# Kernel tuning notes

Measured on AMD Instinct MI355X. Metric: run time of the kernel, lower is better.

Reference implementation:

```python
import jax, jax.numpy as jnp
import numpy as np

SIGMA = 3.0
TRUNCATE = 4.0          # scipy gaussian_filter default
THRESH = 0.01           # thresh_map_after_gaussian_filter
WIN = 5                 # weighted-average window
OFFSET = 0.4395         # offset_due_to_upsampling
SCORE_THRESH = 0.8


def _conv2d(x4, k4, pad):
    # x4: [M,1,H,W], k4: [1,1,kh,kw], pad: ((ph,ph),(pw,pw)) zero padding
    return jax.lax.conv_general_dilated(
        x4, k4, window_strides=(1, 1), padding=pad,
        dimension_numbers=('NCHW', 'OIHW', 'NCHW'))


def _gaussian_filter(x4):
    # scipy.ndimage.gaussian_filter(sigma=3, mode='reflect') == separable conv
    # with symmetric (edge-mirrored) padding, radius = int(truncate*sigma+0.5)
    r = int(TRUNCATE * SIGMA + 0.5)  # 12 -> 25-tap kernel
    t = jnp.arange(-r, r + 1, dtype=x4.dtype)
    k = jnp.exp(-(t * t) / (2.0 * SIGMA * SIGMA))
    k = k / k.sum()
    # along H
    xp = jnp.pad(x4, ((0, 0), (0, 0), (r, r), (0, 0)), mode='symmetric')
    x4 = _conv2d(xp, k.reshape(1, 1, -1, 1), ((0, 0), (0, 0)))
    # along W
    xp = jnp.pad(x4, ((0, 0), (0, 0), (0, 0), (r, r)), mode='symmetric')
    return _conv2d(xp, k.reshape(1, 1, 1, -1), ((0, 0), (0, 0)))


def setup_inputs() -> dict:
    key = jax.random.key(0)
    belief_maps = jax.random.uniform(key, (32, 16, 256, 256), dtype=jnp.float32)
    return {"belief_maps": belief_maps}


def reference(belief_maps):
    B, N, H, W = belief_maps.shape
    M = B * N
    m_ori = belief_maps.reshape(M, 1, H, W)

    # 1) gaussian smoothing for NMS
    g = _gaussian_filter(m_ori)[:, 0]  # [M,H,W]

    # 2) 4-neighbor local-maximum test (zero borders, exactly as numpy shifts)
    up    = jnp.pad(g, ((0, 0), (1, 0), (0, 0)))[:, :H, :]   # g[i-1,j], 0 at top
    down  = jnp.pad(g, ((0, 0), (0, 1), (0, 0)))[:, 1:, :]   # g[i+1,j], 0 at bottom
    left  = jnp.pad(g, ((0, 0), (0, 0), (1, 0)))[:, :, :W]   # g[i,j-1], 0 at left
    right = jnp.pad(g, ((0, 0), (0, 0), (0, 1)))[:, :, 1:]   # g[i,j+1], 0 at right
    peaks = (g >= up) & (g >= down) & (g >= left) & (g >= right) & (g > THRESH)

    # 3) weighted 5x5 window averages over the ORIGINAL map (zero-weight OOB)
    rows = jnp.arange(H, dtype=belief_maps.dtype)[:, None]
    cols = jnp.arange(W, dtype=belief_maps.dtype)[None, :]
    box = jnp.ones((1, 1, WIN, WIN), belief_maps.dtype)
    pad = ((WIN // 2, WIN // 2), (WIN // 2, WIN // 2))
    S  = _conv2d(m_ori, box, pad)[:, 0]                 # sum of weights
    SY = _conv2d(m_ori * rows, box, pad)[:, 0]          # sum(row * w)
    SX = _conv2d(m_ori * cols, box, pad)[:, 0]          # sum(col * w)

    m = m_ori[:, 0]
    neg_inf = jnp.array(-jnp.inf, belief_maps.dtype)
    masked = jnp.where(peaks, m, neg_inf).reshape(M, H * W)
    idx = jnp.argmax(masked, axis=1)                    # best-scoring peak per map
    npk = peaks.reshape(M, H * W).sum(axis=1)           # number of peaks

    def _take(a):
        return jnp.take_along_axis(a.reshape(M, H * W), idx[:, None], axis=1)[:, 0]

    score = _take(m)
    Ssum = _take(S)
    row_p = (idx // W).astype(belief_maps.dtype)
    col_p = (idx % W).astype(belief_maps.dtype)
    safe = jnp.where(Ssum == 0, jnp.ones_like(Ssum), Ssum)
    # try/except fallback to raw peak coords when all window weights are zero
    x = jnp.where(Ssum == 0, col_p, _take(SX) / safe) + OFFSET
    y = jnp.where(Ssum == 0, row_p, _take(SY) / safe) + OFFSET

    # single peak -> always valid; multiple peaks -> top score must be >= 0.8
    valid = (npk == 1) | ((npk > 1) & (score >= SCORE_THRESH))
    kx = jnp.where(valid, x, jnp.full_like(x, -999.999))
    ky = jnp.where(valid, y, jnp.full_like(y, -999.999))
    conf = valid.astype(belief_maps.dtype)
    return jnp.stack([kx, ky, conf], axis=-1).reshape(B, N, 3)
```

## Files before the change

kernel.cpp:

```cpp
#include <hip/hip_runtime.h>
#include <cmath>

#define HH 256
#define WW 256
#define RAD 12
#define KLEN 25
#define NMAPS 512
#define ESTRIP 32
#define NSTRIP (HH / ESTRIP)
#define RING 29

typedef float v2f __attribute__((ext_vector_type(2)));

__global__ __launch_bounds__(256) void blur_peak_strip(
    const float* __restrict__ in,
    float* __restrict__ sval,
    int* __restrict__ sidx,
    int* __restrict__ scnt)
{
    __shared__ __align__(16) float vrow[4][2][WW + 2 * RAD];

    const int tid  = threadIdx.x;
    const int l    = tid & 63;
    const int wv   = tid >> 6;
    const int sid  = blockIdx.x * 4 + wv;
    const int m     = sid >> 3;
    const int strip = sid & 7;
    const float4* map4 = reinterpret_cast<const float4*>(in) + (size_t)m * (HH * WW / 4);

    const int e0 = strip * ESTRIP;
    const int o0 = e0 - 1;

    float kf[KLEN];
    {
        float s = 0.f; float h[RAD + 1];
#pragma unroll
        for (int i = 0; i <= RAD; ++i) {
            float tt = (float)(i - RAD);
            h[i] = expf(-(tt * tt) / 18.0f);
            s += (i < RAD) ? 2.f * h[i] : h[i];
        }
#pragma unroll
        for (int i = 0; i <= RAD; ++i) h[i] /= s;
#pragma unroll
        for (int i = 0; i < KLEN; ++i) kf[i] = h[(i <= RAD) ? i : (2 * RAD - i)];
    }

    v2f rxy[RING], rzw[RING];
#pragma unroll
    for (int i = 0; i < RING; ++i) {
        int q = o0 + i - RAD;
        int r = (q < 0) ? (-q - 1) : q;
        float4 t4 = map4[(size_t)r * (WW / 4) + l];
        rxy[i] = (v2f){t4.x, t4.y};
        rzw[i] = (v2f){t4.z, t4.w};
    }

    float4 g0v  = make_float4(0.f, 0.f, 0.f, 0.f);
    float4 gm1v = g0v, gm2v = g0v;
    float bval = -1.f;
    int   bidx = 0x7FFFFFFF;
    int   cnt  = 0;
    float4 pf0, pf1, pf2, pf3, pf4;

#define PREFETCH(TT)                                                          \
    {                                                                         \
        int rb = o0 + 5 * (TT) + 17;                                          \
        int r0 = rb, r1 = rb + 1, r2 = rb + 2, r3 = rb + 3, r4 = rb + 4;      \
        if (r0 > HH - 1) r0 = 2 * HH - 1 - r0;                                \
        if (r1 > HH - 1) r1 = 2 * HH - 1 - r1;                                \
        if (r2 > HH - 1) r2 = 2 * HH - 1 - r2;                                \
        if (r3 > HH - 1) r3 = 2 * HH - 1 - r3;                                \
        if (r4 > HH - 1) r4 = 2 * HH - 1 - r4;                                \
        pf0 = map4[(size_t)r0 * (WW / 4) + l];                                \
        pf1 = map4[(size_t)r1 * (WW / 4) + l];                                \
        pf2 = map4[(size_t)r2 * (WW / 4) + l];                                \
        pf3 = map4[(size_t)r3 * (WW / 4) + l];                                \
        pf4 = map4[(size_t)r4 * (WW / 4) + l];                                \
    }

#define ROTATE()                                                              \
    {                                                                         \
        _Pragma("unroll")                                                     \
        for (int i = 0; i < RING - 5; ++i) {                                  \
            rxy[i] = rxy[i + 5]; rzw[i] = rzw[i + 5];                         \
        }                                                                     \
        rxy[24] = (v2f){pf0.x, pf0.y}; rzw[24] = (v2f){pf0.z, pf0.w};         \
        rxy[25] = (v2f){pf1.x, pf1.y}; rzw[25] = (v2f){pf1.z, pf1.w};         \
        rxy[26] = (v2f){pf2.x, pf2.y}; rzw[26] = (v2f){pf2.z, pf2.w};         \
        rxy[27] = (v2f){pf3.x, pf3.y}; rzw[27] = (v2f){pf3.z, pf3.w};         \
        rxy[28] = (v2f){pf4.x, pf4.y}; rzw[28] = (v2f){pf4.z, pf4.w};         \
    }

#define VCW(PP, TP)                                                           \
    {                                                                         \
        v2f vxyA = (v2f){0.f, 0.f}, vxyB = (v2f){0.f, 0.f};                   \
        v2f vzwA = (v2f){0.f, 0.f}, vzwB = (v2f){0.f, 0.f};                   \
        _Pragma("unroll")                                                     \
        for (int d = 0; d < KLEN; d += 2) {                                   \
            vxyA += kf[d] * rxy[(PP) + d];                                    \
            vzwA += kf[d] * rzw[(PP) + d];                                    \
        }                                                                     \
        _Pragma("unroll")                                                     \
        for (int d = 1; d < KLEN; d += 2) {                                   \
            vxyB += kf[d] * rxy[(PP) + d];                                    \
            vzwB += kf[d] * rzw[(PP) + d];                                    \
        }                                                                     \
        v2f vxy = vxyA + vxyB;                                                \
        v2f vzw = vzwA + vzwB;                                                \
        float* wb = vrow[wv][(TP) & 1];                                       \
        reinterpret_cast<float4*>(wb + RAD)[l] =                              \
            make_float4(vxy.x, vxy.y, vzw.x, vzw.y);                          \
        if (l < 3)   reinterpret_cast<float4*>(wb)[2 - l]   =                 \
            make_float4(vzw.y, vzw.x, vxy.y, vxy.x);                          \
        if (l >= 61) reinterpret_cast<float4*>(wb)[130 - l] =                 \
            make_float4(vzw.y, vzw.x, vxy.y, vxy.x);                          \
    }

#define HC()                                                                  \
    {                                                                         \
        float acc0 = 0.f, acc1 = 0.f, acc2 = 0.f, acc3 = 0.f;                 \
        const float4 rda[7] = {rd0, rd1, rd2, rd3, rd4, rd5, rd6};            \
        _Pragma("unroll")                                                     \
        for (int k = 0; k < 7; ++k) {                                         \
            _Pragma("unroll")                                                 \
            for (int e = 0; e < 4; ++e) {                                     \
                const int i = 4 * k + e;                                      \
                const float wval = (e == 0) ? rda[k].x : (e == 1) ? rda[k].y  \
                                 : (e == 2) ? rda[k].z : rda[k].w;            \
                if (i <= 24)           acc0 += kf[i]     * wval;              \
                if (i >= 1 && i <= 25) acc1 += kf[i - 1] * wval;              \
                if (i >= 2 && i <= 26) acc2 += kf[i - 2] * wval;              \
                if (i >= 3)            acc3 += kf[i - 3] * wval;              \
            }                                                                 \
        }                                                                     \
        gm2v = gm1v; gm1v = g0v;                                              \
        g0v = make_float4(acc0, acc1, acc2, acc3);                            \
    }

#define EV(SLOT, EROW)                                                        \
    {                                                                         \
        const int erow = (EROW);                                              \
        float lf0 = __shfl_up(gm1v.w, 1);   if (l == 0)  lf0 = 0.f;           \
        float rt3 = __shfl_down(gm1v.x, 1); if (l == 63) rt3 = 0.f;           \
        const bool etop = (erow == 0), ebot = (erow == HH - 1);               \
        const float gm1a[4] = {gm1v.x, gm1v.y, gm1v.z, gm1v.w};               \
        const float gm2a[4] = {gm2v.x, gm2v.y, gm2v.z, gm2v.w};               \
        const float g0a[4]  = {g0v.x,  g0v.y,  g0v.z,  g0v.w};                \
        const float mva[4]  = {rxy[SLOT].x, rxy[SLOT].y,                      \
                               rzw[SLOT].x, rzw[SLOT].y};                     \
        _Pragma("unroll")                                                     \
        for (int q = 0; q < 4; ++q) {                                         \
            float gE = gm1a[q];                                               \
            float up = etop ? 0.f : gm2a[q];                                  \
            float dn = ebot ? 0.f : g0a[q];                                   \
            float lf = (q == 0) ? lf0 : gm1a[q - 1];                          \
            float rt = (q == 3) ? rt3 : gm1a[q + 1];                          \
            float mx = fmaxf(fmaxf(up, dn), fmaxf(lf, rt));                   \
            bool pk = (gE >= mx) && (gE > 0.01f);                             \
            cnt += pk ? 1 : 0;                                                \
            float mv = mva[q];                                                \
            int fi = erow * WW + 4 * l + q;                                   \
            bool upd = pk && (mv > bval);                                     \
            bval = upd ? mv : bval;                                           \
            bidx = upd ? fi : bidx;                                           \
        }                                                                     \
    }

#define ROW_FULL(TB, PP)                                                      \
    {                                                                         \
        const int tpar = ((TB) + (PP)) & 1;      \
        const float4* rb4 =                                                   \
            reinterpret_cast<const float4*>(vrow[wv][tpar ^ 1]);              \
        float4 rd0 = rb4[l + 0], rd1 = rb4[l + 1], rd2 = rb4[l + 2],          \
               rd3 = rb4[l + 3], rd4 = rb4[l + 4], rd5 = rb4[l + 5],          \
               rd6 = rb4[l + 6];                                              \
        VCW(PP, tpar);                                                        \
        __builtin_amdgcn_wave_barrier();                                      \
        HC();                                                                 \
        EV((PP) + 10, o0 + 5 * (TB) + (PP) - 2);                              \
    }

#define ROW_NOEV(PP)                                                          \
    {                                                                         \
        const int tpar = (PP) & 1;                                            \
        const float4* rb4 =                                                   \
            reinterpret_cast<const float4*>(vrow[wv][tpar ^ 1]);              \
        float4 rd0 = rb4[l + 0], rd1 = rb4[l + 1], rd2 = rb4[l + 2],          \
               rd3 = rb4[l + 3], rd4 = rb4[l + 4], rd5 = rb4[l + 5],          \
               rd6 = rb4[l + 6];                                              \
        VCW(PP, PP);                                                          \
        __builtin_amdgcn_wave_barrier();                                      \
        HC();                                                                 \
    }

    PREFETCH(0);
    VCW(0, 0);
    __builtin_amdgcn_wave_barrier();
    ROW_NOEV(1);
    ROW_NOEV(2);
    ROW_FULL(0, 3);
    ROW_FULL(0, 4);
    ROTATE();

#pragma unroll 1
    for (int T = 1; T < 6; ++T) {
        PREFETCH(T);
        ROW_FULL(T, 0);
        ROW_FULL(T, 1);
        ROW_FULL(T, 2);
        ROW_FULL(T, 3);
        ROW_FULL(T, 4);
        ROTATE();
    }

    ROW_FULL(6, 0);
    ROW_FULL(6, 1);
    ROW_FULL(6, 2);
    ROW_FULL(6, 3);
    {
        const float4* rb4 = reinterpret_cast<const float4*>(vrow[wv][1]);
        float4 rd0 = rb4[l + 0], rd1 = rb4[l + 1], rd2 = rb4[l + 2],
               rd3 = rb4[l + 3], rd4 = rb4[l + 4], rd5 = rb4[l + 5],
               rd6 = rb4[l + 6];
        HC();
        EV(14, o0 + 32);
    }

#undef ROW_NOEV
#undef ROW_FULL
#undef EV
#undef HC
#undef VCW
#undef ROTATE
#undef PREFETCH

#pragma unroll
    for (int off = 32; off > 0; off >>= 1) {
        float v2 = __shfl_xor(bval, off);
        int   i2 = __shfl_xor(bidx, off);
        int   c2 = __shfl_xor(cnt,  off);
        if (v2 > bval || (v2 == bval && i2 < bidx)) { bval = v2; bidx = i2; }
        cnt += c2;
    }
    if (l == 0) { sval[sid] = bval; sidx[sid] = bidx; scnt[sid] = cnt; }
}

__global__ __launch_bounds__(256) void finalize_kernel(
    const float* __restrict__ in,
    const float* __restrict__ sval,
    const int* __restrict__ sidx,
    const int* __restrict__ scnt,
    float* __restrict__ out)
{
    int t = blockIdx.x * blockDim.x + threadIdx.x;
    if (t >= NMAPS) return;

    float BV = -1.f; int BI = 0x7FFFFFFF; int C = 0;
#pragma unroll
    for (int s2 = 0; s2 < NSTRIP; ++s2) {
        int k = t * NSTRIP + s2;
        float v = sval[k]; int i = sidx[k];
        if (v > BV || (v == BV && i < BI)) { BV = v; BI = i; }
        C += scnt[k];
    }

    bool valid = (C == 1) || ((C > 1) && (BV >= 0.8f));

    float kx = -999.999f, ky = -999.999f, conf = 0.f;
    if (valid) {
        int pr = BI / WW, pc = BI % WW;
        const float* map = in + (size_t)t * HH * WW;
        float S = 0.f, SX = 0.f, SY = 0.f;
#pragma unroll
        for (int dr = -2; dr <= 2; ++dr) {
            int r = pr + dr;
            if (r < 0 || r >= HH) continue;
#pragma unroll
            for (int dc = -2; dc <= 2; ++dc) {
                int cc = pc + dc;
                if (cc < 0 || cc >= WW) continue;
                float mv = map[r * WW + cc];
                S  += mv;
                SX += mv * (float)cc;
                SY += mv * (float)r;
            }
        }
        float x = (S == 0.f) ? (float)pc : (SX / S);
        float y = (S == 0.f) ? (float)pr : (SY / S);
        kx = x + 0.4395f;
        ky = y + 0.4395f;
        conf = 1.f;
    }
    out[t * 3 + 0] = kx;
    out[t * 3 + 1] = ky;
    out[t * 3 + 2] = conf;
}

extern "C" void kernel_launch(void* const* d_in, const int* in_sizes, int n_in,
                              void* d_out, int out_size, void* d_ws, size_t ws_size,
                              hipStream_t stream) {
    const float* in = (const float*)d_in[0];
    float* out = (float*)d_out;

    const int nstrips = NMAPS * NSTRIP;
    float* sval = (float*)d_ws;
    int*   sidx = (int*)((char*)d_ws + (size_t)nstrips * 4);
    int*   scnt = (int*)((char*)d_ws + (size_t)nstrips * 8);

    blur_peak_strip<<<nstrips / 4, 256, 0, stream>>>(in, sval, sidx, scnt);
    finalize_kernel<<<(NMAPS + 255) / 256, 256, 0, stream>>>(in, sval, sidx, scnt, out);
}
```

Baseline: 82.14 us.

## Fuse finalize into strip kernel via atomics and last-arriver reduction

Removes the separate finalize kernel launch by having each strip wave atomically merge its best (value,index) packed into a 64-bit atomicMax and its peak count into per-map counters. The last wave to arrive for a map, detected with an arrival counter, computes the 5x5 weighted centroid using one lane per tap and a wave shuffle reduction, then writes the output. This adds a hipMemsetAsync to clear the workspace, along with global atomics and a threadfence per strip. The risks are atomic contention and a possible mismatch with the reference tie-break ordering.

```diff
diff --git a/kernel.cpp b/kernel.cpp
--- a/kernel.cpp
+++ b/kernel.cpp
@@ -12,11 +12,12 @@
 
 typedef float v2f __attribute__((ext_vector_type(2)));
 
-__global__ __launch_bounds__(256) void blur_peak_strip(
+__global__ __launch_bounds__(256) void blur_peak_fused(
     const float* __restrict__ in,
-    float* __restrict__ sval,
-    int* __restrict__ sidx,
-    int* __restrict__ scnt)
+    unsigned long long* __restrict__ best,
+    unsigned int* __restrict__ npkA,
+    unsigned int* __restrict__ arr,
+    float* __restrict__ out)
 {
     __shared__ __align__(16) float vrow[4][2][WW + 2 * RAD];
 
@@ -169,7 +170,7 @@
 
 #define ROW_FULL(TB, PP)                                                      \
     {                                                                         \
-        const int tpar = ((TB) + (PP)) & 1;      \
+        const int tpar = ((TB) + (PP)) & 1;                                   \
         const float4* rb4 =                                                   \
             reinterpret_cast<const float4*>(vrow[wv][tpar ^ 1]);              \
         float4 rd0 = rb4[l + 0], rd1 = rb4[l + 1], rd2 = rb4[l + 2],          \
@@ -243,58 +244,61 @@
         if (v2 > bval || (v2 == bval && i2 < bidx)) { bval = v2; bidx = i2; }
         cnt += c2;
     }
-    if (l == 0) { sval[sid] = bval; sidx[sid] = bidx; scnt[sid] = cnt; }
-}
-
-__global__ __launch_bounds__(256) void finalize_kernel(
-    const float* __restrict__ in,
-    const float* __restrict__ sval,
-    const int* __restrict__ sidx,
-    const int* __restrict__ scnt,
-    float* __restrict__ out)
-{
-    int t = blockIdx.x * blockDim.x + threadIdx.x;
-    if (t >= NMAPS) return;
-
-    float BV = -1.f; int BI = 0x7FFFFFFF; int C = 0;
-#pragma unroll
-    for (int s2 = 0; s2 < NSTRIP; ++s2) {
-        int k = t * NSTRIP + s2;
-        float v = sval[k]; int i = sidx[k];
-        if (v > BV || (v == BV && i < BI)) { BV = v; BI = i; }
-        C += scnt[k];
-    }
-
-    bool valid = (C == 1) || ((C > 1) && (BV >= 0.8f));
-
-    float kx = -999.999f, ky = -999.999f, conf = 0.f;
-    if (valid) {
-        int pr = BI / WW, pc = BI % WW;
-        const float* map = in + (size_t)t * HH * WW;
-        float S = 0.f, SX = 0.f, SY = 0.f;
-#pragma unroll
-        for (int dr = -2; dr <= 2; ++dr) {
-            int r = pr + dr;
-            if (r < 0 || r >= HH) continue;
-#pragma unroll
-            for (int dc = -2; dc <= 2; ++dc) {
-                int cc = pc + dc;
-                if (cc < 0 || cc >= WW) continue;
-                float mv = map[r * WW + cc];
-                S  += mv;
-                SX += mv * (float)cc;
-                SY += mv * (float)r;
+
+    int last = 0;
+    if (l == 0) {
+        if (cnt > 0) {
+            unsigned long long packed =
+                ((unsigned long long)__float_as_uint(bval) << 32) |
+                (unsigned long long)(~(unsigned int)bidx);
+            atomicMax(&best[m], packed);
+        }
+        atomicAdd(&npkA[m], (unsigned int)cnt);
+        __threadfence();
+        unsigned int old = atomicAdd(&arr[m], 1u);
+        last = (old == NSTRIP - 1) ? 1 : 0;
+    }
+    last = __shfl(last, 0);
+    if (last) {
+        unsigned long long bb = 0; unsigned int C = 0;
+        if (l == 0) {
+            bb = atomicAdd(&best[m], 0ull);
+            C  = atomicAdd(&npkA[m], 0u);
+        }
+        bb = __shfl(bb, 0);
+        C  = __shfl(C, 0);
+
+        float score = __uint_as_float((unsigned int)(bb >> 32));
+        int   fi    = (int)(~(unsigned int)(bb & 0xFFFFFFFFull));
+        bool valid = (C == 1u) || ((C > 1u) && (score >= 0.8f));
+
+        float kx = -999.999f, ky = -999.999f, conf = 0.f;
+        if (valid) {
+            int pr_ = fi >> 8, pc_ = fi & 255;
+            int dr = l / 5 - 2, dc = l % 5 - 2;
+            int rr = pr_ + dr, cc = pc_ + dc;
+            float mv = 0.f;
+            bool inb = (l < 25) && (rr >= 0) && (rr < HH) && (cc >= 0) && (cc < WW);
+            if (inb) mv = reinterpret_cast<const float*>(map4)[rr * WW + cc];
+            float S = mv, SX = mv * (float)cc, SY = mv * (float)rr;
+#pragma unroll
+            for (int off = 32; off > 0; off >>= 1) {
+                S  += __shfl_xor(S,  off);
+                SX += __shfl_xor(SX, off);
+                SY += __shfl_xor(SY, off);
             }
-        }
-        float x = (S == 0.f) ? (float)pc : (SX / S);
-        float y = (S == 0.f) ? (float)pr : (SY / S);
-        kx = x + 0.4395f;
-        ky = y + 0.4395f;
-        conf = 1.f;
-    }
-    out[t * 3 + 0] = kx;
-    out[t * 3 + 1] = ky;
-    out[t * 3 + 2] = conf;
+            float x = (S == 0.f) ? (float)pc_ : (SX / S);
+            float y = (S == 0.f) ? (float)pr_ : (SY / S);
+            kx = x + 0.4395f;
+            ky = y + 0.4395f;
+            conf = 1.f;
+        }
+        if (l == 0) {
+            out[m * 3 + 0] = kx;
+            out[m * 3 + 1] = ky;
+            out[m * 3 + 2] = conf;
+        }
+    }
 }
 
 extern "C" void kernel_launch(void* const* d_in, const int* in_sizes, int n_in,
@@ -303,11 +307,12 @@
     const float* in = (const float*)d_in[0];
     float* out = (float*)d_out;
 
+    unsigned long long* best = (unsigned long long*)d_ws;
+    unsigned int* npkA = (unsigned int*)((char*)d_ws + NMAPS * 8);
+    unsigned int* arr  = (unsigned int*)((char*)d_ws + NMAPS * 8 + NMAPS * 4);
+
+    hipMemsetAsync(d_ws, 0, NMAPS * 16, stream);
+
     const int nstrips = NMAPS * NSTRIP;
-    float* sval = (float*)d_ws;
-    int*   sidx = (int*)((char*)d_ws + (size_t)nstrips * 4);
-    int*   scnt = (int*)((char*)d_ws + (size_t)nstrips * 8);
-
-    blur_peak_strip<<<nstrips / 4, 256, 0, stream>>>(in, sval, sidx, scnt);
-    finalize_kernel<<<(NMAPS + 255) / 256, 256, 0, stream>>>(in, sval, sidx, scnt, out);
+    blur_peak_fused<<<nstrips / 4, 256, 0, stream>>>(in, best, npkA, arr, out);
 }
```

Measured after the change: 163.2 us. 98.7% more time.
